# Kernel tuning notes

Measured on AMD Instinct MI355X. Metric: run time of the kernel, lower is better.

The kernel has to match this reference:

```python
import jax, jax.numpy as jnp
import numpy as np

N, E, DIN, D, FE, L, B, M = 10000, 40000, 11, 64, 4, 4, 512, 3


def setup_inputs() -> dict:
    key = jax.random.key(0)
    ks = iter(jax.random.split(key, 24))
    s = lambda *sh: jax.random.normal(next(ks), sh, jnp.float32)
    return {
        "x": s(N, DIN),
        "edge_index": jax.random.randint(next(ks), (2, E), 0, N),
        "edge_attr": jax.random.uniform(next(ks), (E, FE), jnp.float32),
        "batch": jnp.sort(jax.random.randint(next(ks), (N,), 0, B)),
        "W0": s(DIN, D) * 0.1, "b0": jnp.zeros((D,), jnp.float32),
        "Wn1": s(FE, 2 * D) * 0.1, "bn1": jnp.zeros((2 * D,), jnp.float32),
        "Wn2": s(2 * D, D * D) * 0.02, "bn2": jnp.zeros((D * D,), jnp.float32),
        "root": s(L, D, D) * 0.1, "conv_bias": jnp.zeros((L, D), jnp.float32),
        "lstm_Wih": s(4 * D, 2 * D) * 0.1, "lstm_Whh": s(4 * D, D) * 0.1,
        "lstm_b": jnp.zeros((4 * D,), jnp.float32),
        "Wo1": s(2 * D, D) * 0.1, "bo1": jnp.zeros((D,), jnp.float32),
        "Wo2": s(D, 1) * 0.1, "bo2": jnp.zeros((1,), jnp.float32),
    }


def reference(x, edge_index, edge_attr, batch, W0, b0, Wn1, bn1, Wn2, bn2,
              root, conv_bias, lstm_Wih, lstm_Whh, lstm_b, Wo1, bo1, Wo2, bo2):
    src, dst = edge_index[0], edge_index[1]
    h = x @ W0 + b0  # [N, D]
    # Edge MLP is SHARED across all conv layers -> compute per-edge weight matrices once
    ew = (jax.nn.silu(edge_attr @ Wn1 + bn1) @ Wn2 + bn2).reshape(E, D, D)
    for l in range(L):
        msg = jnp.einsum('ed,edf->ef', h[src], ew)  # gather-compute per edge
        aggr = jax.ops.segment_sum(msg, dst, num_segments=N)  # scatter-add to targets
        h = h + (aggr + h @ root[l] + conv_bias[l])  # NNConv + residual
    # Set2Set pooling (LSTM, M processing steps)
    q_star = jnp.zeros((B, 2 * D), h.dtype)
    hs = jnp.zeros((B, D), h.dtype)
    cs = jnp.zeros((B, D), h.dtype)
    for _ in range(M):
        gates = q_star @ lstm_Wih.T + hs @ lstm_Whh.T + lstm_b
        i, f, g, o = jnp.split(gates, 4, axis=-1)  # torch LSTM gate order
        cs = jax.nn.sigmoid(f) * cs + jax.nn.sigmoid(i) * jnp.tanh(g)
        hs = jax.nn.sigmoid(o) * jnp.tanh(cs)
        q = hs  # [B, D]
        e = jnp.sum(h * q[batch], axis=-1)  # [N]
        emax = jax.ops.segment_max(e, batch, num_segments=B)
        ex = jnp.exp(e - emax[batch])
        denom = jax.ops.segment_sum(ex, batch, num_segments=B)
        a = ex / denom[batch]  # per-graph softmax attention
        r = jax.ops.segment_sum(a[:, None] * h, batch, num_segments=B)
        q_star = jnp.concatenate([q, r], axis=-1)
    out = jax.nn.silu(q_star @ Wo1 + bo1) @ Wo2 + bo2
    return out.reshape(-1)
```

## Files before the change

### kernel.cpp

```cpp
#include <hip/hip_runtime.h>
#include <cstdint>
#include <cstddef>

#define NN   10000
#define EE   40000
#define DIN_ 11
#define DD   64
#define LL   4
#define BB   512
#define MM   3
#define K1   128
#define DD2  4096
#define NPB  16
#define NCH  8
#define CSPL 2
#define CPB  4
#define ESLOT 12
#define ECREG (8 * ESLOT)

typedef unsigned short ushort_t;
typedef unsigned int   uint_t;

typedef __bf16 bf16x8_t __attribute__((ext_vector_type(8)));
typedef float  f32x4_t  __attribute__((ext_vector_type(4)));
union FragU { uint4 u; bf16x8_t b; };

__device__ __forceinline__ float bfu(ushort_t u) { return __uint_as_float(((uint_t)u) << 16); }
__device__ __forceinline__ float bflo(uint_t u) { return __uint_as_float(u << 16); }
__device__ __forceinline__ float bfhi(uint_t u) { return __uint_as_float(u & 0xffff0000u); }
__device__ __forceinline__ ushort_t f2bf(float f) {
  uint_t u = __float_as_uint(f);
  u = (u + 0x7fffu + ((u >> 16) & 1u)) >> 16;
  return (ushort_t)u;
}
__device__ __forceinline__ uint_t pack2(float lo, float hi) {
  return (uint_t)f2bf(lo) | ((uint_t)f2bf(hi) << 16);
}
__device__ __forceinline__ float sigmf_(float x) { return 1.f / (1.f + expf(-x)); }
__device__ __forceinline__ float siluf_(float x) { return x / (1.f + expf(-x)); }

#if defined(__HIP_DEVICE_COMPILE__) && __has_builtin(__builtin_amdgcn_fdot2_f32_bf16)
typedef __bf16 bf16x2_t __attribute__((ext_vector_type(2)));
__device__ __forceinline__ float dot2a(uint_t a, uint_t b, float c) {
  union { uint_t u; bf16x2_t v; } ua, ub;
  ua.u = a; ub.u = b;
  return __builtin_amdgcn_fdot2_f32_bf16(ua.v, ub.v, c, false);
}
#else
__device__ __forceinline__ float dot2a(uint_t a, uint_t b, float c) {
  return c + bflo(a) * bflo(b) + bfhi(a) * bfhi(b);
}
#endif

#define NCANON 16
struct CanonArgs {
  const void* src[NCANON];
  float* dst[NCANON];
  int n[NCANON];
};
__global__ void k_canon(CanonArgs a, const ushort_t* __restrict__ ea, int* __restrict__ flag) {
  __shared__ int bad;
  if (threadIdx.x == 0) bad = 0;
  __syncthreads();
  ushort_t u = ea[threadIdx.x];
  if ((u & 0x8000u) || u > 0x3F80u) atomicAdd(&bad, 1);
  __syncthreads();
  const int isbf = (bad == 0) ? 1 : 0;
  if (blockIdx.x == 0 && blockIdx.y == 0 && threadIdx.x == 0) *flag = isbf;
  const int ai = blockIdx.y;
  const int n = a.n[ai];
  const int i = blockIdx.x * 256 + threadIdx.x;
  if (i >= n) return;
  float v;
  if (isbf) v = bfu(((const ushort_t*)a.src[ai])[i]);
  else      v = ((const float*)a.src[ai])[i];
  a.dst[ai][i] = v;
}

__global__ void k_wn2m(const void* __restrict__ Wn2, uint_t* __restrict__ out,
                       const int* __restrict__ flag) {
  __shared__ ushort_t row[DD2];
  const int k = blockIdx.x, tid = threadIdx.x;
  if (*flag) {
    const uint4* src = (const uint4*)((const ushort_t*)Wn2 + (size_t)k * DD2);
    ((uint4*)row)[tid] = src[tid];
    ((uint4*)row)[tid + 256] = src[tid + 256];
  } else {
    const float* src = (const float*)Wn2 + (size_t)k * DD2;
    for (int j = 0; j < 16; ++j) row[tid + 256 * j] = f2bf(src[tid + 256 * j]);
  }
  __syncthreads();
  const int kpg = k >> 1, par = k & 1;
  const int lane = tid >> 2, jp = tid & 3;
  const int q = lane >> 4, n = lane & 15;
  for (int fc = 0; fc < 4; ++fc) {
#pragma unroll
    for (int hf = 0; hf < 2; ++hf) {
      int d0 = hf * 32 + q * 8 + 2 * jp;
      int f = fc * 16 + n;
      uint_t lo = row[d0 * 64 + f], hi = row[(d0 + 1) * 64 + f];
      out[((((size_t)kpg * 4 + fc) * 2 + par) * 2 + hf) * 256 + tid] = lo | (hi << 16);
    }
  }
}

__global__ void k_wT(const float* __restrict__ Wihc, const float* __restrict__ Whhc,
                     float* __restrict__ Wiht, float* __restrict__ Whht) {
  int idx = blockIdx.x * 256 + threadIdx.x;
  if (idx < 4 * DD * K1) {
    int j = idx >> 7, i = idx & 127;
    Wiht[i * 256 + j] = Wihc[idx];
  }
  if (idx < 4 * DD * DD) {
    int j = idx >> 6, i = idx & 63;
    Whht[i * 256 + j] = Whhc[idx];
  }
}

__global__ void k_embed(const float* __restrict__ x, const float* __restrict__ W0,
                        const float* __restrict__ b0, const float* __restrict__ bn2,
                        float* __restrict__ h, uint_t* __restrict__ hpk,
                        float* __restrict__ nbias) {
  __shared__ float xs[DIN_];
  __shared__ float hl[DD];
  const int n = blockIdx.x, f = threadIdx.x;
  if (f < DIN_) xs[f] = x[n * DIN_ + f];
  __syncthreads();
  float a = b0[f];
  for (int i = 0; i < DIN_; ++i) a += xs[i] * W0[i * DD + f];
  h[(size_t)n * DD + f] = a;
  hl[f] = a;
  float other = __shfl_down(a, 1);
  if ((f & 1) == 0)
    hpk[(size_t)n * 32 + (f >> 1)] = pack2(a, other);
  __syncthreads();
  float nb = 0.f;
#pragma unroll
  for (int d = 0; d < DD; ++d) nb += hl[d] * bn2[d * DD + f];
  nbias[(size_t)n * DD + f] = nb;
}

__global__ void k_edgemlp(const float* __restrict__ ea, const float* __restrict__ Wn1,
                          const float* __restrict__ bn1, const int* __restrict__ epos,
                          uint_t* __restrict__ hn1c) {
  int idx = blockIdx.x * 256 + threadIdx.x;
  if (idx >= EE * (K1 / 2)) return;
  int e = idx >> 6, j = idx & 63;
  int k0 = 2 * j, k1 = 2 * j + 1;
  float a0 = ea[e * 4 + 0], a1 = ea[e * 4 + 1], a2 = ea[e * 4 + 2], a3 = ea[e * 4 + 3];
  float t0 = bn1[k0] + a0 * Wn1[k0] + a1 * Wn1[K1 + k0] + a2 * Wn1[2 * K1 + k0] + a3 * Wn1[3 * K1 + k0];
  float t1 = bn1[k1] + a0 * Wn1[k1] + a1 * Wn1[K1 + k1] + a2 * Wn1[2 * K1 + k1] + a3 * Wn1[3 * K1 + k1];
  int pos = epos[e];
  hn1c[((size_t)(j >> 3) * EE + pos) * 8 + (j & 7)] = pack2(siluf_(t0), siluf_(t1));
}

__global__ void k_hist(const int* __restrict__ ei, int* __restrict__ cnt_s) {
  int e = blockIdx.x * 256 + threadIdx.x;
  if (e >= EE) return;
  atomicAdd(&cnt_s[ei[e]], 1);
}

__global__ void k_scan(const int* __restrict__ cnt, int* __restrict__ rp,
                       const int* __restrict__ batch, int* __restrict__ goff) {
  if (blockIdx.x == 1) {
    int g = threadIdx.x;
    if (g > BB) return;
    int lo = 0, hi = NN;
    while (lo < hi) {
      int mid = (lo + hi) >> 1;
      if (batch[mid] < g) lo = mid + 1; else hi = mid;
    }
    goff[g] = lo;
    return;
  }
  __shared__ int part[1024];
  const int tid = threadIdx.x;
  const int chunk = (NN + 1023) / 1024;
  int s = 0;
  for (int j = 0; j < chunk; ++j) {
    int idx = tid * chunk + j;
    if (idx < NN) s += cnt[idx];
  }
  part[tid] = s;
  __syncthreads();
  for (int off = 1; off < 1024; off <<= 1) {
    int v = (tid >= off) ? part[tid - off] : 0;
    __syncthreads();
    part[tid] += v;
    __syncthreads();
  }
  int base = (tid == 0) ? 0 : part[tid - 1];
  for (int j = 0; j < chunk; ++j) {
    int idx = tid * chunk + j;
    if (idx < NN) { rp[idx] = base; base += cnt[idx]; }
  }
  if (tid == 1023) rp[NN] = part[1023];
}

__global__ void k_fill(const int* __restrict__ ei, const int* __restrict__ rps,
                       int* __restrict__ cur_s, int* __restrict__ epos,
                       int* __restrict__ esd) {
  int e = blockIdx.x * 256 + threadIdx.x;
  if (e >= EE) return;
  int s = ei[e], d = ei[EE + e];
  int ps = atomicAdd(&cur_s[s], 1);
  int pos = rps[s] + ps;
  epos[e] = pos;
  esd[2 * pos] = s;
  esd[2 * pos + 1] = d;
}

__global__ __launch_bounds__(512, 4) void k_conv(
    const uint_t* __restrict__ hpk, const uint_t* __restrict__ hn1c,
    const uint_t* __restrict__ Wn2m, const float* __restrict__ nbias,
    const int* __restrict__ rps, const int* __restrict__ esd,
    float* __restrict__ aggr) {
  __shared__ uint_t Gp[NPB * 2 * 64 * 4];
  __shared__ int2 eStage[ECREG];
  const int tid = threadIdx.x;
  const int w = tid >> 6, lane = tid & 63;
  const int q = lane >> 4, n16 = lane & 15;
  const int half = blockIdx.x / 625;
  const int ng = blockIdx.x - half * 625;
  const int n0 = ng * NPB;
  const int e0 = rps[n0], e1 = rps[n0 + NPB];
  const int ecnt = e1 - e0;

  if (tid < ECREG && tid < ecnt) eStage[tid] = ((const int2*)esd)[e0 + tid];

  FragU a0, a1;
  {
    const uint4* ap = (const uint4*)(hpk + (size_t)(n0 + n16) * 32);
    a0.u = ap[q];
    a1.u = ap[4 + q];
  }
  __syncthreads();

  float acc[ESLOT];
#pragma unroll
  for (int s = 0; s < ESLOT; ++s) {
    const int li = w + 8 * s;
    float v = 0.f;
    if (half == 0 && li < ecnt && li < ECREG)
      v = nbias[(size_t)eStage[li].x * 64 + lane];
    acc[s] = v;
  }

  const int kq = w >> 2, slot = w & 3;
  for (int cc = 0; cc < CPB; ++cc) {
    const int c = half * CPB + cc;
    if (cc) __syncthreads();
    const int kpg = c * 8 + w;
    for (int fc = 0; fc < 4; ++fc) {
      const uint4* bp = (const uint4*)Wn2m + (size_t)(kpg * 4 + fc) * 256 + lane;
      FragU b00, b01, b10, b11;
      b00.u = bp[0];
      b01.u = bp[64];
      b10.u = bp[128];
      b11.u = bp[192];
      f32x4_t acc0 = {0.f, 0.f, 0.f, 0.f};
      f32x4_t acc1 = {0.f, 0.f, 0.f, 0.f};
      acc0 = __builtin_amdgcn_mfma_f32_16x16x32_bf16(a0.b, b00.b, acc0, 0, 0, 0);
      acc0 = __builtin_amdgcn_mfma_f32_16x16x32_bf16(a1.b, b01.b, acc0, 0, 0, 0);
      acc1 = __builtin_amdgcn_mfma_f32_16x16x32_bf16(a0.b, b10.b, acc1, 0, 0, 0);
      acc1 = __builtin_amdgcn_mfma_f32_16x16x32_bf16(a1.b, b11.b, acc1, 0, 0, 0);
#pragma unroll
      for (int r = 0; r < 4; ++r) {
        const int m = q * 4 + r;
        Gp[(((m * 2 + kq) * 64 + fc * 16 + n16) * 4 + slot)] = pack2(acc0[r], acc1[r]);
      }
    }
    __syncthreads();
#pragma unroll
    for (int s = 0; s < ESLOT; ++s) {
      const int li = w + 8 * s;
      if (li < ecnt && li < ECREG) {
        const int2 sd = eStage[li];
        const int m = sd.x - n0;
        const uint4* hp = (const uint4*)(hn1c + ((size_t)c * EE + e0 + li) * 8);
        uint4 hv0 = hp[0], hv1 = hp[1];
        const uint4* gb = (const uint4*)Gp + (size_t)(m * 2) * 64 + lane;
        uint4 g0 = gb[0], g1 = gb[64];
        float p = acc[s];
        p = dot2a(g0.x, hv0.x, p);
        p = dot2a(g0.y, hv0.y, p);
        p = dot2a(g0.z, hv0.z, p);
        p = dot2a(g0.w, hv0.w, p);
        p = dot2a(g1.x, hv1.x, p);
        p = dot2a(g1.y, hv1.y, p);
        p = dot2a(g1.z, hv1.z, p);
        p = dot2a(g1.w, hv1.w, p);
        acc[s] = p;
      }
    }
    for (int li = ECREG + w; li < ecnt; li += 8) {
      const int ii = e0 + li;
      const int src = __builtin_amdgcn_readfirstlane(esd[2 * ii]);
      const int dst = __builtin_amdgcn_readfirstlane(esd[2 * ii + 1]);
      const int m = src - n0;
      float p = (half == 0 && cc == 0) ? nbias[(size_t)src * 64 + lane] : 0.f;
      const uint4* hp = (const uint4*)(hn1c + ((size_t)c * EE + ii) * 8);
      uint4 hv0 = hp[0], hv1 = hp[1];
      const uint4* gb = (const uint4*)Gp + (size_t)(m * 2) * 64 + lane;
      uint4 g0 = gb[0], g1 = gb[64];
      p = dot2a(g0.x, hv0.x, p);
      p = dot2a(g0.y, hv0.y, p);
      p = dot2a(g0.z, hv0.z, p);
      p = dot2a(g0.w, hv0.w, p);
      p = dot2a(g1.x, hv1.x, p);
      p = dot2a(g1.y, hv1.y, p);
      p = dot2a(g1.z, hv1.z, p);
      p = dot2a(g1.w, hv1.w, p);
      atomicAdd(&aggr[(size_t)dst * 64 + lane], p);
    }
  }
#pragma unroll
  for (int s = 0; s < ESLOT; ++s) {
    const int li = w + 8 * s;
    if (li < ecnt && li < ECREG) {
      const int dst = eStage[li].y;
      atomicAdd(&aggr[(size_t)dst * 64 + lane], acc[s]);
    }
  }
}

__global__ __launch_bounds__(256) void k_update(
    float* __restrict__ h, uint_t* __restrict__ hpk,
    float* __restrict__ aggr, const float* __restrict__ bn2,
    const float* __restrict__ root, const float* __restrict__ cb,
    float* __restrict__ nbias, int l) {
  __shared__ float hl[4][DD];
  __shared__ float al[4][DD];
  const int tid = threadIdx.x, w = tid >> 6, f = tid & 63;
  const int n = blockIdx.x * 4 + w;
  float hv = h[(size_t)n * DD + f];
  hl[w][f] = hv;
  float acc = hv + aggr[(size_t)n * DD + f] + cb[l * DD + f];
  aggr[(size_t)n * DD + f] = 0.f;
  __syncthreads();
  const float* rp = root + (size_t)l * DD2;
#pragma unroll
  for (int d = 0; d < DD; ++d) acc += hl[w][d] * rp[d * DD + f];
  h[(size_t)n * DD + f] = acc;
  al[w][f] = acc;
  float other = __shfl_down(acc, 1);
  if ((f & 1) == 0)
    hpk[(size_t)n * 32 + (f >> 1)] = pack2(acc, other);
  __syncthreads();
  float nb = 0.f;
#pragma unroll
  for (int d = 0; d < DD; ++d) nb += al[w][d] * bn2[d * DD + f];
  nbias[(size_t)n * DD + f] = nb;
}

#define EVCAP 2048
__global__ void k_s2s(const float* __restrict__ h, const int* __restrict__ goff,
                      const float* __restrict__ Wiht, const float* __restrict__ Whht,
                      const float* __restrict__ lb,
                      const float* __restrict__ Wo1, const float* __restrict__ bo1,
                      const float* __restrict__ Wo2, const float* __restrict__ bo2,
                      void* __restrict__ outv, const int* __restrict__ flag) {
  __shared__ float qsl[K1];
  __shared__ float hsl[DD];
  __shared__ float csl[DD];
  __shared__ float gl[4][DD];
  __shared__ float red[256];
  __shared__ float ev[EVCAP];
  __shared__ float rp4[4][DD];
  const int g = blockIdx.x, tid = threadIdx.x;

  if (tid < K1) qsl[tid] = 0.f;
  else if (tid < K1 + DD) hsl[tid - K1] = 0.f;
  else csl[tid - K1 - DD] = 0.f;
  __syncthreads();

  const int i0 = goff[g];
  int cnt = goff[g + 1] - i0;
  if (cnt > EVCAP) cnt = EVCAP;

  for (int m = 0; m < MM; ++m) {
    {
      float a = lb[tid];
      for (int i = 0; i < K1; ++i) a += qsl[i] * Wiht[i * 256 + tid];
      for (int i = 0; i < DD; ++i) a += hsl[i] * Whht[i * 256 + tid];
      gl[tid >> 6][tid & 63] = a;
    }
    __syncthreads();
    if (tid < DD) {
      float ig = sigmf_(gl[0][tid]), fg = sigmf_(gl[1][tid]);
      float gg = tanhf(gl[2][tid]), og = sigmf_(gl[3][tid]);
      float c = fg * csl[tid] + ig * gg;
      csl[tid] = c;
      hsl[tid] = og * tanhf(c);
    }
    __syncthreads();
    float lmax = -1e30f;
    for (int jj = tid; jj < cnt; jj += 256) {
      const float* hp = h + (size_t)(i0 + jj) * DD;
      float e = 0.f;
#pragma unroll
      for (int d = 0; d < DD; ++d) e += hp[d] * hsl[d];
      ev[jj] = e;
      lmax = fmaxf(lmax, e);
    }
    red[tid] = lmax;
    __syncthreads();
    for (int s = 128; s > 0; s >>= 1) {
      if (tid < s) red[tid] = fmaxf(red[tid], red[tid + s]);
      __syncthreads();
    }
    const float emax = red[0];
    __syncthreads();
    float lsum = 0.f;
    for (int jj = tid; jj < cnt; jj += 256) {
      float ex = expf(ev[jj] - emax);
      ev[jj] = ex;
      lsum += ex;
    }
    red[tid] = lsum;
    __syncthreads();
    for (int s = 128; s > 0; s >>= 1) {
      if (tid < s) red[tid] += red[tid + s];
      __syncthreads();
    }
    const float denom = red[0];
    const int f = tid & 63, grp = tid >> 6;
    float acc = 0.f;
    for (int jj = grp; jj < cnt; jj += 4)
      acc += ev[jj] * h[(size_t)(i0 + jj) * DD + f];
    rp4[grp][f] = acc;
    __syncthreads();
    if (tid < DD) {
      float r = rp4[0][tid] + rp4[1][tid] + rp4[2][tid] + rp4[3][tid];
      r = (cnt > 0 && denom > 0.f) ? r / denom : 0.f;
      qsl[tid] = hsl[tid];
      qsl[DD + tid] = r;
    }
    __syncthreads();
  }
  if (tid < DD) {
    float t = bo1[tid];
    for (int i = 0; i < K1; ++i) t += qsl[i] * Wo1[i * DD + tid];
    float s = siluf_(t) * Wo2[tid];
    for (int off = 32; off > 0; off >>= 1) s += __shfl_down(s, off);
    if (tid == 0) {
      float v = s + bo2[0];
      if (*flag) ((ushort_t*)outv)[g] = f2bf(v);
      else       ((float*)outv)[g] = v;
    }
  }
}

extern "C" void kernel_launch(void* const* d_in, const int* in_sizes, int n_in,
                              void* d_out, int out_size, void* d_ws, size_t ws_size,
                              hipStream_t stream) {
  const void* x_r    = d_in[0];
  const int*  ei     = (const int*)d_in[1];
  const void* ea_r   = d_in[2];
  const int*  batch  = (const int*)d_in[3];
  const void* W0_r   = d_in[4];
  const void* b0_r   = d_in[5];
  const void* Wn1_r  = d_in[6];
  const void* bn1_r  = d_in[7];
  const void* Wn2_r  = d_in[8];
  const void* bn2_r  = d_in[9];
  const void* root_r = d_in[10];
  const void* cb_r   = d_in[11];
  const void* Wih_r  = d_in[12];
  const void* Whh_r  = d_in[13];
  const void* lb_r   = d_in[14];
  const void* Wo1_r  = d_in[15];
  const void* bo1_r  = d_in[16];
  const void* Wo2_r  = d_in[17];
  const void* bo2_r  = d_in[18];

  char* w = (char*)d_ws;
  size_t off = 0;
  auto alloc = [&](size_t bytes) -> void* {
    void* p = w + off;
    off = (off + bytes + 255) & ~(size_t)255;
    return p;
  };
  int* flag = (int*)alloc(4);
  float* xc    = (float*)alloc((size_t)NN * DIN_ * 4);
  float* eac   = (float*)alloc((size_t)EE * 4 * 4);
  float* W0c   = (float*)alloc((size_t)DIN_ * DD * 4);
  float* b0c   = (float*)alloc((size_t)DD * 4);
  float* Wn1c  = (float*)alloc((size_t)4 * K1 * 4);
  float* bn1c  = (float*)alloc((size_t)K1 * 4);
  float* bn2c  = (float*)alloc((size_t)DD2 * 4);
  float* rootc = (float*)alloc((size_t)LL * DD2 * 4);
  float* cbc   = (float*)alloc((size_t)LL * DD * 4);
  float* Wihc  = (float*)alloc((size_t)4 * DD * K1 * 4);
  float* Whhc  = (float*)alloc((size_t)4 * DD * DD * 4);
  float* lbc   = (float*)alloc((size_t)4 * DD * 4);
  float* Wo1c  = (float*)alloc((size_t)K1 * DD * 4);
  float* bo1c  = (float*)alloc((size_t)DD * 4);
  float* Wo2c  = (float*)alloc((size_t)DD * 4);
  float* bo2c  = (float*)alloc((size_t)4);
  float* Wiht  = (float*)alloc((size_t)K1 * 256 * 4);
  float* Whht  = (float*)alloc((size_t)DD * 256 * 4);
  uint_t* Wn2m = (uint_t*)alloc((size_t)64 * 4 * 2 * 2 * 64 * 4 * 4);
  float*  h    = (float*)alloc((size_t)NN * DD * 4);
  uint_t* hpk  = (uint_t*)alloc((size_t)NN * 32 * 4);
  uint_t* hn1c = (uint_t*)alloc((size_t)EE * (K1 / 2) * 4);
  float*  aggr = (float*)alloc((size_t)NN * DD * 4);
  float*  nbias= (float*)alloc((size_t)NN * DD * 4);
  int* cnts  = (int*)alloc((size_t)2 * NN * 4);
  int* rps   = (int*)alloc((size_t)(NN + 1) * 4);
  int* epos  = (int*)alloc((size_t)EE * 4);
  int* esd   = (int*)alloc((size_t)2 * EE * 4);
  int* goff  = (int*)alloc((size_t)(BB + 1) * 4);

  int* cnt_s = cnts;
  int* cur_s = cnts + NN;

  hipMemsetAsync(cnts, 0, (size_t)2 * NN * 4, stream);
  hipMemsetAsync(aggr, 0, (size_t)NN * DD * 4, stream);

  CanonArgs ca;
  const void* srcs[NCANON] = {x_r, ea_r, W0_r, b0_r, Wn1_r, bn1_r, bn2_r, root_r,
                              cb_r, Wih_r, Whh_r, lb_r, Wo1_r, bo1_r, Wo2_r, bo2_r};
  float* dsts[NCANON] = {xc, eac, W0c, b0c, Wn1c, bn1c, bn2c, rootc,
                         cbc, Wihc, Whhc, lbc, Wo1c, bo1c, Wo2c, bo2c};
  int cnts_c[NCANON] = {NN * DIN_, EE * 4, DIN_ * DD, DD, 4 * K1, K1, DD2, LL * DD2,
                        LL * DD, 4 * DD * K1, 4 * DD * DD, 4 * DD, K1 * DD, DD, DD, 1};
  for (int i = 0; i < NCANON; ++i) { ca.src[i] = srcs[i]; ca.dst[i] = dsts[i]; ca.n[i] = cnts_c[i]; }
  {
    dim3 grid((EE * 4 + 255) / 256, NCANON);
    k_canon<<<grid, 256, 0, stream>>>(ca, (const ushort_t*)ea_r, flag);
  }
  k_wn2m<<<K1, 256, 0, stream>>>(Wn2_r, Wn2m, flag);
  k_wT<<<(4 * DD * K1 + 255) / 256, 256, 0, stream>>>(Wihc, Whhc, Wiht, Whht);

  k_embed<<<NN, DD, 0, stream>>>(xc, W0c, b0c, bn2c, h, hpk, nbias);
  k_hist<<<(EE + 255) / 256, 256, 0, stream>>>(ei, cnt_s);
  k_scan<<<2, 1024, 0, stream>>>(cnt_s, rps, batch, goff);
  k_fill<<<(EE + 255) / 256, 256, 0, stream>>>(ei, rps, cur_s, epos, esd);
  k_edgemlp<<<(EE * (K1 / 2) + 255) / 256, 256, 0, stream>>>(eac, Wn1c, bn1c, epos, hn1c);

  for (int l = 0; l < LL; ++l) {
    k_conv<<<CSPL * (NN / NPB), 512, 0, stream>>>(hpk, hn1c, Wn2m, nbias, rps, esd, aggr);
    k_update<<<NN / 4, 256, 0, stream>>>(h, hpk, aggr, bn2c, rootc, cbc, nbias, l);
  }

  k_s2s<<<BB, 256, 0, stream>>>(h, goff, Wiht, Whht, lbc, Wo1c, bo1c, Wo2c, bo2c,
                                d_out, flag);
}
```

Measured before the change: 462.9 us.

## Fuse prep kernels, drop canonicalization copies, and pad conv shared-memory stride

Removes the separate canonicalization kernel that copied every input to fp32 and instead detects bf16 inline with a wave ballot, reading raw inputs through a dtype-aware loader. The Wn2 reorder, LSTM weight transpose, node embedding (now 4 nodes per block) and edge-count histogram are merged into one multi-role prep kernel. The conv kernel's shared staging buffer gets a padded row stride to reduce bank conflicts, and the s2s shared event buffer shrinks. The cost is a detection check repeated in every kernel and per-element type branching in the inner loops.

```diff
diff --git a/kernel.cpp b/kernel.cpp
--- a/kernel.cpp
+++ b/kernel.cpp
@@ -12,11 +12,11 @@
 #define K1   128
 #define DD2  4096
 #define NPB  16
-#define NCH  8
 #define CSPL 2
 #define CPB  4
 #define ESLOT 12
 #define ECREG (8 * ESLOT)
+#define GSTR 516
 
 typedef unsigned short ushort_t;
 typedef unsigned int   uint_t;
@@ -52,112 +52,85 @@
 }
 #endif
 
-#define NCANON 16
-struct CanonArgs {
-  const void* src[NCANON];
-  float* dst[NCANON];
-  int n[NCANON];
-};
-__global__ void k_canon(CanonArgs a, const ushort_t* __restrict__ ea, int* __restrict__ flag) {
-  __shared__ int bad;
-  if (threadIdx.x == 0) bad = 0;
-  __syncthreads();
-  ushort_t u = ea[threadIdx.x];
-  if ((u & 0x8000u) || u > 0x3F80u) atomicAdd(&bad, 1);
-  __syncthreads();
-  const int isbf = (bad == 0) ? 1 : 0;
-  if (blockIdx.x == 0 && blockIdx.y == 0 && threadIdx.x == 0) *flag = isbf;
-  const int ai = blockIdx.y;
-  const int n = a.n[ai];
-  const int i = blockIdx.x * 256 + threadIdx.x;
-  if (i >= n) return;
-  float v;
-  if (isbf) v = bfu(((const ushort_t*)a.src[ai])[i]);
-  else      v = ((const float*)a.src[ai])[i];
-  a.dst[ai][i] = v;
-}
-
-__global__ void k_wn2m(const void* __restrict__ Wn2, uint_t* __restrict__ out,
-                       const int* __restrict__ flag) {
+__device__ __forceinline__ int detect_bf16(const void* ea) {
+  const int lane = threadIdx.x & 63;
+  uint_t v = ((const uint_t*)ea)[lane];
+  ushort_t a = (ushort_t)(v & 0xffffu), b = (ushort_t)(v >> 16);
+  bool bad = (a & 0x8000u) || a > 0x3F80u || (b & 0x8000u) || b > 0x3F80u;
+  return __ballot(bad) == 0ull ? 1 : 0;
+}
+__device__ __forceinline__ float ldf(const void* p, size_t i, int isbf) {
+  return isbf ? bfu(((const ushort_t*)p)[i]) : ((const float*)p)[i];
+}
+
+__global__ __launch_bounds__(256) void k_prep(
+    const void* __restrict__ ea, const void* __restrict__ Wn2, uint_t* __restrict__ wn2m,
+    const void* __restrict__ Wih, const void* __restrict__ Whh,
+    float* __restrict__ Wiht, float* __restrict__ Whht,
+    const void* __restrict__ x, const void* __restrict__ W0, const void* __restrict__ b0,
+    const void* __restrict__ bn2, float* __restrict__ h, uint_t* __restrict__ hpk,
+    float* __restrict__ nbias,
+    const int* __restrict__ ei, int* __restrict__ cnt_s) {
   __shared__ ushort_t row[DD2];
-  const int k = blockIdx.x, tid = threadIdx.x;
-  if (*flag) {
-    const uint4* src = (const uint4*)((const ushort_t*)Wn2 + (size_t)k * DD2);
-    ((uint4*)row)[tid] = src[tid];
-    ((uint4*)row)[tid + 256] = src[tid + 256];
+  __shared__ float xs4[4][DIN_];
+  __shared__ float hl4[4][DD];
+  const int bx = blockIdx.x, tid = threadIdx.x;
+  const int isbf = detect_bf16(ea);
+
+  if (bx < 128) {
+    const int k = bx;
+    if (isbf) {
+      const uint4* src = (const uint4*)((const ushort_t*)Wn2 + (size_t)k * DD2);
+      ((uint4*)row)[tid] = src[tid];
+      ((uint4*)row)[tid + 256] = src[tid + 256];
+    } else {
+      const float* src = (const float*)Wn2 + (size_t)k * DD2;
+      for (int j = 0; j < 16; ++j) row[tid + 256 * j] = f2bf(src[tid + 256 * j]);
+    }
+    __syncthreads();
+    const int kpg = k >> 1, par = k & 1;
+    const int lane = tid >> 2, jp = tid & 3;
+    const int q = lane >> 4, n = lane & 15;
+    for (int fc = 0; fc < 4; ++fc) {
+#pragma unroll
+      for (int hf = 0; hf < 2; ++hf) {
+        int d0 = hf * 32 + q * 8 + 2 * jp;
+        int f = fc * 16 + n;
+        uint_t lo = row[d0 * 64 + f], hi = row[(d0 + 1) * 64 + f];
+        wn2m[((((size_t)kpg * 4 + fc) * 2 + par) * 2 + hf) * 256 + tid] = lo | (hi << 16);
+      }
+    }
+  } else if (bx < 256) {
+    int idx = (bx - 128) * 256 + tid;
+    {
+      int j = idx >> 7, i = idx & 127;
+      Wiht[i * 256 + j] = ldf(Wih, idx, isbf);
+    }
+    if (idx < 4 * DD * DD) {
+      int j = idx >> 6, i = idx & 63;
+      Whht[i * 256 + j] = ldf(Whh, idx, isbf);
+    }
+  } else if (bx < 256 + NN / 4) {
+    const int w = tid >> 6, f = tid & 63;
+    const int n = (bx - 256) * 4 + w;
+    if (f < DIN_) xs4[w][f] = ldf(x, (size_t)n * DIN_ + f, isbf);
+    __syncthreads();
+    float a = ldf(b0, f, isbf);
+    for (int i = 0; i < DIN_; ++i) a += xs4[w][i] * ldf(W0, i * DD + f, isbf);
+    h[(size_t)n * DD + f] = a;
+    hl4[w][f] = a;
+    float other = __shfl_down(a, 1);
+    if ((f & 1) == 0)
+      hpk[(size_t)n * 32 + (f >> 1)] = pack2(a, other);
+    __syncthreads();
+    float nb = 0.f;
+#pragma unroll
+    for (int d = 0; d < DD; ++d) nb += hl4[w][d] * ldf(bn2, d * DD + f, isbf);
+    nbias[(size_t)n * DD + f] = nb;
   } else {
-    const float* src = (const float*)Wn2 + (size_t)k * DD2;
-    for (int j = 0; j < 16; ++j) row[tid + 256 * j] = f2bf(src[tid + 256 * j]);
-  }
-  __syncthreads();
-  const int kpg = k >> 1, par = k & 1;
-  const int lane = tid >> 2, jp = tid & 3;
-  const int q = lane >> 4, n = lane & 15;
-  for (int fc = 0; fc < 4; ++fc) {
-#pragma unroll
-    for (int hf = 0; hf < 2; ++hf) {
-      int d0 = hf * 32 + q * 8 + 2 * jp;
-      int f = fc * 16 + n;
-      uint_t lo = row[d0 * 64 + f], hi = row[(d0 + 1) * 64 + f];
-      out[((((size_t)kpg * 4 + fc) * 2 + par) * 2 + hf) * 256 + tid] = lo | (hi << 16);
-    }
-  }
-}
-
-__global__ void k_wT(const float* __restrict__ Wihc, const float* __restrict__ Whhc,
-                     float* __restrict__ Wiht, float* __restrict__ Whht) {
-  int idx = blockIdx.x * 256 + threadIdx.x;
-  if (idx < 4 * DD * K1) {
-    int j = idx >> 7, i = idx & 127;
-    Wiht[i * 256 + j] = Wihc[idx];
-  }
-  if (idx < 4 * DD * DD) {
-    int j = idx >> 6, i = idx & 63;
-    Whht[i * 256 + j] = Whhc[idx];
-  }
-}
-
-__global__ void k_embed(const float* __restrict__ x, const float* __restrict__ W0,
-                        const float* __restrict__ b0, const float* __restrict__ bn2,
-                        float* __restrict__ h, uint_t* __restrict__ hpk,
-                        float* __restrict__ nbias) {
-  __shared__ float xs[DIN_];
-  __shared__ float hl[DD];
-  const int n = blockIdx.x, f = threadIdx.x;
-  if (f < DIN_) xs[f] = x[n * DIN_ + f];
-  __syncthreads();
-  float a = b0[f];
-  for (int i = 0; i < DIN_; ++i) a += xs[i] * W0[i * DD + f];
-  h[(size_t)n * DD + f] = a;
-  hl[f] = a;
-  float other = __shfl_down(a, 1);
-  if ((f & 1) == 0)
-    hpk[(size_t)n * 32 + (f >> 1)] = pack2(a, other);
-  __syncthreads();
-  float nb = 0.f;
-#pragma unroll
-  for (int d = 0; d < DD; ++d) nb += hl[d] * bn2[d * DD + f];
-  nbias[(size_t)n * DD + f] = nb;
-}
-
-__global__ void k_edgemlp(const float* __restrict__ ea, const float* __restrict__ Wn1,
-                          const float* __restrict__ bn1, const int* __restrict__ epos,
-                          uint_t* __restrict__ hn1c) {
-  int idx = blockIdx.x * 256 + threadIdx.x;
-  if (idx >= EE * (K1 / 2)) return;
-  int e = idx >> 6, j = idx & 63;
-  int k0 = 2 * j, k1 = 2 * j + 1;
-  float a0 = ea[e * 4 + 0], a1 = ea[e * 4 + 1], a2 = ea[e * 4 + 2], a3 = ea[e * 4 + 3];
-  float t0 = bn1[k0] + a0 * Wn1[k0] + a1 * Wn1[K1 + k0] + a2 * Wn1[2 * K1 + k0] + a3 * Wn1[3 * K1 + k0];
-  float t1 = bn1[k1] + a0 * Wn1[k1] + a1 * Wn1[K1 + k1] + a2 * Wn1[2 * K1 + k1] + a3 * Wn1[3 * K1 + k1];
-  int pos = epos[e];
-  hn1c[((size_t)(j >> 3) * EE + pos) * 8 + (j & 7)] = pack2(siluf_(t0), siluf_(t1));
-}
-
-__global__ void k_hist(const int* __restrict__ ei, int* __restrict__ cnt_s) {
-  int e = blockIdx.x * 256 + threadIdx.x;
-  if (e >= EE) return;
-  atomicAdd(&cnt_s[ei[e]], 1);
+    int e = (bx - 256 - NN / 4) * 256 + tid;
+    if (e < EE) atomicAdd(&cnt_s[ei[e]], 1);
+  }
 }
 
 __global__ void k_scan(const int* __restrict__ cnt, int* __restrict__ rp,
@@ -210,12 +183,30 @@
   esd[2 * pos + 1] = d;
 }
 
+__global__ void k_edgemlp(const void* __restrict__ ea, const void* __restrict__ Wn1,
+                          const void* __restrict__ bn1, const int* __restrict__ epos,
+                          uint_t* __restrict__ hn1c) {
+  const int isbf = detect_bf16(ea);
+  int idx = blockIdx.x * 256 + threadIdx.x;
+  if (idx >= EE * (K1 / 2)) return;
+  int e = idx >> 6, j = idx & 63;
+  int k0 = 2 * j, k1 = 2 * j + 1;
+  float a0 = ldf(ea, e * 4 + 0, isbf), a1 = ldf(ea, e * 4 + 1, isbf);
+  float a2 = ldf(ea, e * 4 + 2, isbf), a3 = ldf(ea, e * 4 + 3, isbf);
+  float t0 = ldf(bn1, k0, isbf) + a0 * ldf(Wn1, k0, isbf) + a1 * ldf(Wn1, K1 + k0, isbf)
+           + a2 * ldf(Wn1, 2 * K1 + k0, isbf) + a3 * ldf(Wn1, 3 * K1 + k0, isbf);
+  float t1 = ldf(bn1, k1, isbf) + a0 * ldf(Wn1, k1, isbf) + a1 * ldf(Wn1, K1 + k1, isbf)
+           + a2 * ldf(Wn1, 2 * K1 + k1, isbf) + a3 * ldf(Wn1, 3 * K1 + k1, isbf);
+  int pos = epos[e];
+  hn1c[((size_t)(j >> 3) * EE + pos) * 8 + (j & 7)] = pack2(siluf_(t0), siluf_(t1));
+}
+
 __global__ __launch_bounds__(512, 4) void k_conv(
     const uint_t* __restrict__ hpk, const uint_t* __restrict__ hn1c,
     const uint_t* __restrict__ Wn2m, const float* __restrict__ nbias,
     const int* __restrict__ rps, const int* __restrict__ esd,
     float* __restrict__ aggr) {
-  __shared__ uint_t Gp[NPB * 2 * 64 * 4];
+  __shared__ uint_t Gp[NPB * GSTR];
   __shared__ int2 eStage[ECREG];
   const int tid = threadIdx.x;
   const int w = tid >> 6, lane = tid & 63;
@@ -267,7 +258,7 @@
 #pragma unroll
       for (int r = 0; r < 4; ++r) {
         const int m = q * 4 + r;
-        Gp[(((m * 2 + kq) * 64 + fc * 16 + n16) * 4 + slot)] = pack2(acc0[r], acc1[r]);
+        Gp[(size_t)m * GSTR + (kq * 64 + fc * 16 + n16) * 4 + slot] = pack2(acc0[r], acc1[r]);
       }
     }
     __syncthreads();
@@ -279,7 +270,7 @@
         const int m = sd.x - n0;
         const uint4* hp = (const uint4*)(hn1c + ((size_t)c * EE + e0 + li) * 8);
         uint4 hv0 = hp[0], hv1 = hp[1];
-        const uint4* gb = (const uint4*)Gp + (size_t)(m * 2) * 64 + lane;
+        const uint4* gb = (const uint4*)Gp + (size_t)m * (GSTR / 4) + lane;
         uint4 g0 = gb[0], g1 = gb[64];
         float p = acc[s];
         p = dot2a(g0.x, hv0.x, p);
@@ -301,7 +292,7 @@
       float p = (half == 0 && cc == 0) ? nbias[(size_t)src * 64 + lane] : 0.f;
       const uint4* hp = (const uint4*)(hn1c + ((size_t)c * EE + ii) * 8);
       uint4 hv0 = hp[0], hv1 = hp[1];
-      const uint4* gb = (const uint4*)Gp + (size_t)(m * 2) * 64 + lane;
+      const uint4* gb = (const uint4*)Gp + (size_t)m * (GSTR / 4) + lane;
       uint4 g0 = gb[0], g1 = gb[64];
       p = dot2a(g0.x, hv0.x, p);
       p = dot2a(g0.y, hv0.y, p);
@@ -325,22 +316,24 @@
 }
 
 __global__ __launch_bounds__(256) void k_update(
+    const void* __restrict__ ea,
     float* __restrict__ h, uint_t* __restrict__ hpk,
-    float* __restrict__ aggr, const float* __restrict__ bn2,
-    const float* __restrict__ root, const float* __restrict__ cb,
+    float* __restrict__ aggr, const void* __restrict__ bn2,
+    const void* __restrict__ root, const void* __restrict__ cb,
     float* __restrict__ nbias, int l) {
   __shared__ float hl[4][DD];
   __shared__ float al[4][DD];
+  const int isbf = detect_bf16(ea);
   const int tid = threadIdx.x, w = tid >> 6, f = tid & 63;
   const int n = blockIdx.x * 4 + w;
   float hv = h[(size_t)n * DD + f];
   hl[w][f] = hv;
-  float acc = hv + aggr[(size_t)n * DD + f] + cb[l * DD + f];
+  float acc = hv + aggr[(size_t)n * DD + f] + ldf(cb, l * DD + f, isbf);
   aggr[(size_t)n * DD + f] = 0.f;
   __syncthreads();
-  const float* rp = root + (size_t)l * DD2;
-#pragma unroll
-  for (int d = 0; d < DD; ++d) acc += hl[w][d] * rp[d * DD + f];
+  const size_t rbase = (size_t)l * DD2;
+#pragma unroll
+  for (int d = 0; d < DD; ++d) acc += hl[w][d] * ldf(root, rbase + d * DD + f, isbf);
   h[(size_t)n * DD + f] = acc;
   al[w][f] = acc;
   float other = __shfl_down(acc, 1);
@@ -349,17 +342,18 @@
   __syncthreads();
   float nb = 0.f;
 #pragma unroll
-  for (int d = 0; d < DD; ++d) nb += al[w][d] * bn2[d * DD + f];
+  for (int d = 0; d < DD; ++d) nb += al[w][d] * ldf(bn2, d * DD + f, isbf);
   nbias[(size_t)n * DD + f] = nb;
 }
 
-#define EVCAP 2048
-__global__ void k_s2s(const float* __restrict__ h, const int* __restrict__ goff,
+#define EVCAP 512
+__global__ void k_s2s(const void* __restrict__ ea,
+                      const float* __restrict__ h, const int* __restrict__ goff,
                       const float* __restrict__ Wiht, const float* __restrict__ Whht,
-                      const float* __restrict__ lb,
-                      const float* __restrict__ Wo1, const float* __restrict__ bo1,
-                      const float* __restrict__ Wo2, const float* __restrict__ bo2,
-                      void* __restrict__ outv, const int* __restrict__ flag) {
+                      const void* __restrict__ lb,
+                      const void* __restrict__ Wo1, const void* __restrict__ bo1,
+                      const void* __restrict__ Wo2, const void* __restrict__ bo2,
+                      void* __restrict__ outv) {
   __shared__ float qsl[K1];
   __shared__ float hsl[DD];
   __shared__ float csl[DD];
@@ -367,6 +361,7 @@
   __shared__ float red[256];
   __shared__ float ev[EVCAP];
   __shared__ float rp4[4][DD];
+  const int isbf = detect_bf16(ea);
   const int g = blockIdx.x, tid = threadIdx.x;
 
   if (tid < K1) qsl[tid] = 0.f;
@@ -380,7 +375,7 @@
 
   for (int m = 0; m < MM; ++m) {
     {
-      float a = lb[tid];
+      float a = ldf(lb, tid, isbf);
       for (int i = 0; i < K1; ++i) a += qsl[i] * Wiht[i * 256 + tid];
       for (int i = 0; i < DD; ++i) a += hsl[i] * Whht[i * 256 + tid];
       gl[tid >> 6][tid & 63] = a;
@@ -439,14 +434,14 @@
     __syncthreads();
   }
   if (tid < DD) {
-    float t = bo1[tid];
-    for (int i = 0; i < K1; ++i) t += qsl[i] * Wo1[i * DD + tid];
-    float s = siluf_(t) * Wo2[tid];
+    float t = ldf(bo1, tid, isbf);
+    for (int i = 0; i < K1; ++i) t += qsl[i] * ldf(Wo1, i * DD + tid, isbf);
+    float s = siluf_(t) * ldf(Wo2, tid, isbf);
     for (int off = 32; off > 0; off >>= 1) s += __shfl_down(s, off);
     if (tid == 0) {
-      float v = s + bo2[0];
-      if (*flag) ((ushort_t*)outv)[g] = f2bf(v);
-      else       ((float*)outv)[g] = v;
+      float v = s + ldf(bo2, 0, isbf);
+      if (isbf) ((ushort_t*)outv)[g] = f2bf(v);
+      else      ((float*)outv)[g] = v;
     }
   }
 }
@@ -481,23 +476,6 @@
     off = (off + bytes + 255) & ~(size_t)255;
     return p;
   };
-  int* flag = (int*)alloc(4);
-  float* xc    = (float*)alloc((size_t)NN * DIN_ * 4);
-  float* eac   = (float*)alloc((size_t)EE * 4 * 4);
-  float* W0c   = (float*)alloc((size_t)DIN_ * DD * 4);
-  float* b0c   = (float*)alloc((size_t)DD * 4);
-  float* Wn1c  = (float*)alloc((size_t)4 * K1 * 4);
-  float* bn1c  = (float*)alloc((size_t)K1 * 4);
-  float* bn2c  = (float*)alloc((size_t)DD2 * 4);
-  float* rootc = (float*)alloc((size_t)LL * DD2 * 4);
-  float* cbc   = (float*)alloc((size_t)LL * DD * 4);
-  float* Wihc  = (float*)alloc((size_t)4 * DD * K1 * 4);
-  float* Whhc  = (float*)alloc((size_t)4 * DD * DD * 4);
-  float* lbc   = (float*)alloc((size_t)4 * DD * 4);
-  float* Wo1c  = (float*)alloc((size_t)K1 * DD * 4);
-  float* bo1c  = (float*)alloc((size_t)DD * 4);
-  float* Wo2c  = (float*)alloc((size_t)DD * 4);
-  float* bo2c  = (float*)alloc((size_t)4);
   float* Wiht  = (float*)alloc((size_t)K1 * 256 * 4);
   float* Whht  = (float*)alloc((size_t)DD * 256 * 4);
   uint_t* Wn2m = (uint_t*)alloc((size_t)64 * 4 * 2 * 2 * 64 * 4 * 4);
@@ -518,32 +496,19 @@
   hipMemsetAsync(cnts, 0, (size_t)2 * NN * 4, stream);
   hipMemsetAsync(aggr, 0, (size_t)NN * DD * 4, stream);
 
-  CanonArgs ca;
-  const void* srcs[NCANON] = {x_r, ea_r, W0_r, b0_r, Wn1_r, bn1_r, bn2_r, root_r,
-                              cb_r, Wih_r, Whh_r, lb_r, Wo1_r, bo1_r, Wo2_r, bo2_r};
-  float* dsts[NCANON] = {xc, eac, W0c, b0c, Wn1c, bn1c, bn2c, rootc,
-                         cbc, Wihc, Whhc, lbc, Wo1c, bo1c, Wo2c, bo2c};
-  int cnts_c[NCANON] = {NN * DIN_, EE * 4, DIN_ * DD, DD, 4 * K1, K1, DD2, LL * DD2,
-                        LL * DD, 4 * DD * K1, 4 * DD * DD, 4 * DD, K1 * DD, DD, DD, 1};
-  for (int i = 0; i < NCANON; ++i) { ca.src[i] = srcs[i]; ca.dst[i] = dsts[i]; ca.n[i] = cnts_c[i]; }
-  {
-    dim3 grid((EE * 4 + 255) / 256, NCANON);
-    k_canon<<<grid, 256, 0, stream>>>(ca, (const ushort_t*)ea_r, flag);
-  }
-  k_wn2m<<<K1, 256, 0, stream>>>(Wn2_r, Wn2m, flag);
-  k_wT<<<(4 * DD * K1 + 255) / 256, 256, 0, stream>>>(Wihc, Whhc, Wiht, Whht);
-
-  k_embed<<<NN, DD, 0, stream>>>(xc, W0c, b0c, bn2c, h, hpk, nbias);
-  k_hist<<<(EE + 255) / 256, 256, 0, stream>>>(ei, cnt_s);
+  const int prep_blocks = 256 + NN / 4 + (EE + 255) / 256;
+  k_prep<<<prep_blocks, 256, 0, stream>>>(
+      ea_r, Wn2_r, Wn2m, Wih_r, Whh_r, Wiht, Whht,
+      x_r, W0_r, b0_r, bn2_r, h, hpk, nbias, ei, cnt_s);
   k_scan<<<2, 1024, 0, stream>>>(cnt_s, rps, batch, goff);
   k_fill<<<(EE + 255) / 256, 256, 0, stream>>>(ei, rps, cur_s, epos, esd);
-  k_edgemlp<<<(EE * (K1 / 2) + 255) / 256, 256, 0, stream>>>(eac, Wn1c, bn1c, epos, hn1c);
+  k_edgemlp<<<(EE * (K1 / 2) + 255) / 256, 256, 0, stream>>>(ea_r, Wn1_r, bn1_r, epos, hn1c);
 
   for (int l = 0; l < LL; ++l) {
     k_conv<<<CSPL * (NN / NPB), 512, 0, stream>>>(hpk, hn1c, Wn2m, nbias, rps, esd, aggr);
-    k_update<<<NN / 4, 256, 0, stream>>>(h, hpk, aggr, bn2c, rootc, cbc, nbias, l);
-  }
-
-  k_s2s<<<BB, 256, 0, stream>>>(h, goff, Wiht, Whht, lbc, Wo1c, bo1c, Wo2c, bo2c,
-                                d_out, flag);
-}
+    k_update<<<NN / 4, 256, 0, stream>>>(ea_r, h, hpk, aggr, bn2_r, root_r, cb_r, nbias, l);
+  }
+
+  k_s2s<<<BB, 256, 0, stream>>>(ea_r, h, goff, Wiht, Whht, lb_r, Wo1_r, bo1_r, Wo2_r,
+                                bo2_r, d_out);
+}
```

Result: slower. 509.2 us (+10.0%).

## Restructure conv edge-to-warp mapping and Gp layout to reuse source-node G rows

Applied to the files above, without the earlier changes.

Each warp now processes a contiguous run of ESLOT edges instead of strided ones, so consecutive edges sharing a source node reuse the already-loaded G fragments from LDS. The Gp shared layout is changed to a per-node stride, and each warp computes two k-groups per f-chunk so it can write packed uint2 stores. The embed kernel is batched to 4 nodes per 256-thread block, and the s2s shared-memory buffer EVCAP is shrunk. Shrinking EVCAP risks correctness for graphs with more than 512 nodes if the buffer has no fallback path.

```diff
diff --git a/kernel.cpp b/kernel.cpp
--- a/kernel.cpp
+++ b/kernel.cpp
@@ -12,11 +12,11 @@
 #define K1   128
 #define DD2  4096
 #define NPB  16
-#define NCH  8
 #define CSPL 2
 #define CPB  4
 #define ESLOT 12
 #define ECREG (8 * ESLOT)
+#define GSTR 512
 
 typedef unsigned short ushort_t;
 typedef unsigned int   uint_t;
@@ -117,26 +117,27 @@
   }
 }
 
-__global__ void k_embed(const float* __restrict__ x, const float* __restrict__ W0,
-                        const float* __restrict__ b0, const float* __restrict__ bn2,
-                        float* __restrict__ h, uint_t* __restrict__ hpk,
-                        float* __restrict__ nbias) {
-  __shared__ float xs[DIN_];
-  __shared__ float hl[DD];
-  const int n = blockIdx.x, f = threadIdx.x;
-  if (f < DIN_) xs[f] = x[n * DIN_ + f];
+__global__ __launch_bounds__(256) void k_embed(
+    const float* __restrict__ x, const float* __restrict__ W0,
+    const float* __restrict__ b0, const float* __restrict__ bn2,
+    float* __restrict__ h, uint_t* __restrict__ hpk, float* __restrict__ nbias) {
+  __shared__ float xs4[4][DIN_];
+  __shared__ float hl4[4][DD];
+  const int tid = threadIdx.x, w = tid >> 6, f = tid & 63;
+  const int n = blockIdx.x * 4 + w;
+  if (f < DIN_) xs4[w][f] = x[(size_t)n * DIN_ + f];
   __syncthreads();
   float a = b0[f];
-  for (int i = 0; i < DIN_; ++i) a += xs[i] * W0[i * DD + f];
+  for (int i = 0; i < DIN_; ++i) a += xs4[w][i] * W0[i * DD + f];
   h[(size_t)n * DD + f] = a;
-  hl[f] = a;
+  hl4[w][f] = a;
   float other = __shfl_down(a, 1);
   if ((f & 1) == 0)
     hpk[(size_t)n * 32 + (f >> 1)] = pack2(a, other);
   __syncthreads();
   float nb = 0.f;
 #pragma unroll
-  for (int d = 0; d < DD; ++d) nb += hl[d] * bn2[d * DD + f];
+  for (int d = 0; d < DD; ++d) nb += hl4[w][d] * bn2[d * DD + f];
   nbias[(size_t)n * DD + f] = nb;
 }
 
@@ -215,7 +216,7 @@
     const uint_t* __restrict__ Wn2m, const float* __restrict__ nbias,
     const int* __restrict__ rps, const int* __restrict__ esd,
     float* __restrict__ aggr) {
-  __shared__ uint_t Gp[NPB * 2 * 64 * 4];
+  __shared__ uint_t Gp[NPB * GSTR];
   __shared__ int2 eStage[ECREG];
   const int tid = threadIdx.x;
   const int w = tid >> 6, lane = tid & 63;
@@ -239,58 +240,74 @@
   float acc[ESLOT];
 #pragma unroll
   for (int s = 0; s < ESLOT; ++s) {
-    const int li = w + 8 * s;
+    const int li = w * ESLOT + s;
     float v = 0.f;
-    if (half == 0 && li < ecnt && li < ECREG)
+    if (half == 0 && li < ecnt)
       v = nbias[(size_t)eStage[li].x * 64 + lane];
     acc[s] = v;
   }
 
-  const int kq = w >> 2, slot = w & 3;
+  const int p = w & 3, fh = w >> 2;
+  const int wkq = p >> 1, slot2 = (p & 1) * 2;
   for (int cc = 0; cc < CPB; ++cc) {
     const int c = half * CPB + cc;
     if (cc) __syncthreads();
-    const int kpg = c * 8 + w;
-    for (int fc = 0; fc < 4; ++fc) {
-      const uint4* bp = (const uint4*)Wn2m + (size_t)(kpg * 4 + fc) * 256 + lane;
-      FragU b00, b01, b10, b11;
-      b00.u = bp[0];
-      b01.u = bp[64];
-      b10.u = bp[128];
-      b11.u = bp[192];
-      f32x4_t acc0 = {0.f, 0.f, 0.f, 0.f};
-      f32x4_t acc1 = {0.f, 0.f, 0.f, 0.f};
-      acc0 = __builtin_amdgcn_mfma_f32_16x16x32_bf16(a0.b, b00.b, acc0, 0, 0, 0);
-      acc0 = __builtin_amdgcn_mfma_f32_16x16x32_bf16(a1.b, b01.b, acc0, 0, 0, 0);
-      acc1 = __builtin_amdgcn_mfma_f32_16x16x32_bf16(a0.b, b10.b, acc1, 0, 0, 0);
-      acc1 = __builtin_amdgcn_mfma_f32_16x16x32_bf16(a1.b, b11.b, acc1, 0, 0, 0);
+#pragma unroll
+    for (int fi = 0; fi < 2; ++fi) {
+      const int fc = fh * 2 + fi;
+      uint_t pk[2][4];
+#pragma unroll
+      for (int kk = 0; kk < 2; ++kk) {
+        const int kpg = c * 8 + 2 * p + kk;
+        const uint4* bp = (const uint4*)Wn2m + (size_t)(kpg * 4 + fc) * 256 + lane;
+        FragU b00, b01, b10, b11;
+        b00.u = bp[0];
+        b01.u = bp[64];
+        b10.u = bp[128];
+        b11.u = bp[192];
+        f32x4_t acc0 = {0.f, 0.f, 0.f, 0.f};
+        f32x4_t acc1 = {0.f, 0.f, 0.f, 0.f};
+        acc0 = __builtin_amdgcn_mfma_f32_16x16x32_bf16(a0.b, b00.b, acc0, 0, 0, 0);
+        acc0 = __builtin_amdgcn_mfma_f32_16x16x32_bf16(a1.b, b01.b, acc0, 0, 0, 0);
+        acc1 = __builtin_amdgcn_mfma_f32_16x16x32_bf16(a0.b, b10.b, acc1, 0, 0, 0);
+        acc1 = __builtin_amdgcn_mfma_f32_16x16x32_bf16(a1.b, b11.b, acc1, 0, 0, 0);
+#pragma unroll
+        for (int r = 0; r < 4; ++r)
+          pk[kk][r] = pack2(acc0[r], acc1[r]);
+      }
 #pragma unroll
       for (int r = 0; r < 4; ++r) {
         const int m = q * 4 + r;
-        Gp[(((m * 2 + kq) * 64 + fc * 16 + n16) * 4 + slot)] = pack2(acc0[r], acc1[r]);
+        uint2 v; v.x = pk[0][r]; v.y = pk[1][r];
+        *(uint2*)&Gp[(size_t)m * GSTR + (wkq * 64 + fc * 16 + n16) * 4 + slot2] = v;
       }
     }
     __syncthreads();
+    int prev_src = -1;
+    uint4 g0, g1;
 #pragma unroll
     for (int s = 0; s < ESLOT; ++s) {
-      const int li = w + 8 * s;
-      if (li < ecnt && li < ECREG) {
+      const int li = w * ESLOT + s;
+      if (li < ecnt) {
         const int2 sd = eStage[li];
-        const int m = sd.x - n0;
+        if (sd.x != prev_src) {
+          prev_src = sd.x;
+          const uint4* gb = (const uint4*)Gp + (size_t)(prev_src - n0) * (GSTR / 4) + lane;
+          g0 = gb[0];
+          g1 = gb[64];
+        }
         const uint4* hp = (const uint4*)(hn1c + ((size_t)c * EE + e0 + li) * 8);
         uint4 hv0 = hp[0], hv1 = hp[1];
-        const uint4* gb = (const uint4*)Gp + (size_t)(m * 2) * 64 + lane;
-        uint4 g0 = gb[0], g1 = gb[64];
-        float p = acc[s];
-        p = dot2a(g0.x, hv0.x, p);
-        p = dot2a(g0.y, hv0.y, p);
-        p = dot2a(g0.z, hv0.z, p);
-        p = dot2a(g0.w, hv0.w, p);
-        p = dot2a(g1.x, hv1.x, p);
-        p = dot2a(g1.y, hv1.y, p);
-        p = dot2a(g1.z, hv1.z, p);
-        p = dot2a(g1.w, hv1.w, p);
-        acc[s] = p;
+        float pt = acc[s];
+        pt = dot2a(g0.x, hv0.x, pt);
+        pt = dot2a(g0.y, hv0.y, pt);
+        pt = dot2a(g0.z, hv0.z, pt);
+        pt = dot2a(g0.w, hv0.w, pt);
+        pt = dot2a(g1.x, hv1.x, pt);
+        pt = dot2a(g1.y, hv1.y, pt);
+        pt = dot2a(g1.z, hv1.z, pt);
+        pt = dot2a(g1.w, hv1.w, pt);
+        acc[s] = pt;
       }
     }
     for (int li = ECREG + w; li < ecnt; li += 8) {
@@ -298,26 +315,26 @@
       const int src = __builtin_amdgcn_readfirstlane(esd[2 * ii]);
       const int dst = __builtin_amdgcn_readfirstlane(esd[2 * ii + 1]);
       const int m = src - n0;
-      float p = (half == 0 && cc == 0) ? nbias[(size_t)src * 64 + lane] : 0.f;
+      float pt = (half == 0 && cc == 0) ? nbias[(size_t)src * 64 + lane] : 0.f;
       const uint4* hp = (const uint4*)(hn1c + ((size_t)c * EE + ii) * 8);
       uint4 hv0 = hp[0], hv1 = hp[1];
-      const uint4* gb = (const uint4*)Gp + (size_t)(m * 2) * 64 + lane;
-      uint4 g0 = gb[0], g1 = gb[64];
-      p = dot2a(g0.x, hv0.x, p);
-      p = dot2a(g0.y, hv0.y, p);
-      p = dot2a(g0.z, hv0.z, p);
-      p = dot2a(g0.w, hv0.w, p);
-      p = dot2a(g1.x, hv1.x, p);
-      p = dot2a(g1.y, hv1.y, p);
-      p = dot2a(g1.z, hv1.z, p);
-      p = dot2a(g1.w, hv1.w, p);
-      atomicAdd(&aggr[(size_t)dst * 64 + lane], p);
+      const uint4* gb = (const uint4*)Gp + (size_t)m * (GSTR / 4) + lane;
+      uint4 og0 = gb[0], og1 = gb[64];
+      pt = dot2a(og0.x, hv0.x, pt);
+      pt = dot2a(og0.y, hv0.y, pt);
+      pt = dot2a(og0.z, hv0.z, pt);
+      pt = dot2a(og0.w, hv0.w, pt);
+      pt = dot2a(og1.x, hv1.x, pt);
+      pt = dot2a(og1.y, hv1.y, pt);
+      pt = dot2a(og1.z, hv1.z, pt);
+      pt = dot2a(og1.w, hv1.w, pt);
+      atomicAdd(&aggr[(size_t)dst * 64 + lane], pt);
     }
   }
 #pragma unroll
   for (int s = 0; s < ESLOT; ++s) {
-    const int li = w + 8 * s;
-    if (li < ecnt && li < ECREG) {
+    const int li = w * ESLOT + s;
+    if (li < ecnt) {
       const int dst = eStage[li].y;
       atomicAdd(&aggr[(size_t)dst * 64 + lane], acc[s]);
     }
@@ -353,7 +370,7 @@
   nbias[(size_t)n * DD + f] = nb;
 }
 
-#define EVCAP 2048
+#define EVCAP 512
 __global__ void k_s2s(const float* __restrict__ h, const int* __restrict__ goff,
                       const float* __restrict__ Wiht, const float* __restrict__ Whht,
                       const float* __restrict__ lb,
@@ -533,7 +550,7 @@
   k_wn2m<<<K1, 256, 0, stream>>>(Wn2_r, Wn2m, flag);
   k_wT<<<(4 * DD * K1 + 255) / 256, 256, 0, stream>>>(Wihc, Whhc, Wiht, Whht);
 
-  k_embed<<<NN, DD, 0, stream>>>(xc, W0c, b0c, bn2c, h, hpk, nbias);
+  k_embed<<<NN / 4, 256, 0, stream>>>(xc, W0c, b0c, bn2c, h, hpk, nbias);
   k_hist<<<(EE + 255) / 256, 256, 0, stream>>>(ei, cnt_s);
   k_scan<<<2, 1024, 0, stream>>>(cnt_s, rps, batch, goff);
   k_fill<<<(EE + 255) / 256, 256, 0, stream>>>(ei, rps, cur_s, epos, esd);
```

Result: slower. 483.7 us (+4.5%).
